# Performance work log

Hardware: AMD Instinct MI355X
Metric: run time of the kernel (lower is better)

Reference implementation:

```python
import jax, jax.numpy as jnp
import numpy as np

B, CIN, COUT, K, SDIM, H, W = 16, 512, 512, 3, 512, 64, 64


def setup_inputs() -> dict:
    key = jax.random.key(0)
    k1, k2, k3, k4 = jax.random.split(key, 4)
    return {
        "x": jax.random.normal(k1, (B, CIN, H, W), dtype=jnp.float32),
        "style": jax.random.normal(k2, (B, SDIM), dtype=jnp.float32),
        "weight": jax.random.normal(k3, (COUT, CIN, K, K), dtype=jnp.float32),
        "style_w": jax.random.normal(k4, (CIN, SDIM), dtype=jnp.float32),
        "style_b": jnp.ones((CIN,), dtype=jnp.float32),  # bias.data.fill_(1.0)
    }


def reference(x, style, weight, style_w, style_b):
    batch, in_ch, h, w_size = x.shape
    out_ch, _, ks, _ = weight.shape
    pad = ks // 2
    # EqualizedLinear: runtime weight scaling by 1/sqrt(fan_in)
    lin_scale = 1.0 / np.sqrt(style_w.shape[1])
    s = style @ (style_w * lin_scale).T + style_b  # [B, Cin]
    # modulate
    conv_scale = 1.0 / np.sqrt(in_ch * ks * ks)
    wmod = (weight[None] * conv_scale) * s[:, None, :, None, None]  # [B,Cout,Cin,k,k]
    # demodulate
    dcoef = jax.lax.rsqrt(jnp.sum(jnp.square(wmod), axis=(2, 3, 4)) + 1e-8)  # [B,Cout]
    wmod = wmod * dcoef[:, :, None, None, None]
    # grouped conv with groups = batch
    x_r = x.reshape(1, batch * in_ch, h, w_size)
    w_r = wmod.reshape(batch * out_ch, in_ch, ks, ks)
    out = jax.lax.conv_general_dilated(
        x_r, w_r,
        window_strides=(1, 1),
        padding=[(pad, pad), (pad, pad)],
        dimension_numbers=("NCHW", "OIHW", "NCHW"),
        feature_group_count=batch,
    )
    return out.reshape(batch, out_ch, h, w_size)
```

## Files before the change

### kernel.cpp

```cpp
#include <hip/hip_runtime.h>
#include <math.h>

#define B 16
#define CIN 512
#define COUT 512
#define SDIM 512
#define H 64
#define W 64

typedef short s16x8 __attribute__((ext_vector_type(8)));
typedef float f32x4 __attribute__((ext_vector_type(4)));

__device__ __constant__ float LIN_SCALE  = 0.04419417382415922f;
__device__ __constant__ float CONV_SCALE = 0.014731391274719742f;

__device__ __forceinline__ ushort f2bf(float f) {
  unsigned u = __float_as_uint(f);
  return (ushort)((u + 0x7FFFu + ((u >> 16) & 1u)) >> 16);
}

#define GLOAD16(g, l)                                           \
  __builtin_amdgcn_global_load_lds(                             \
      (const __attribute__((address_space(1))) unsigned*)(g),   \
      (__attribute__((address_space(3))) unsigned*)(l), 16, 0, 0)

__global__ __launch_bounds__(512) void style_mod_kernel(
    const float* __restrict__ style, const float* __restrict__ style_w,
    const float* __restrict__ style_b, float* __restrict__ s,
    float* __restrict__ s2) {
  const int b = blockIdx.x;
  const int ci = threadIdx.x;
  __shared__ float st[SDIM];
  st[ci] = style[b * SDIM + ci];
  __syncthreads();

  const float4* wr = reinterpret_cast<const float4*>(style_w + (size_t)ci * SDIM);
  float acc = 0.f;
#pragma unroll 4
  for (int k = 0; k < SDIM / 4; ++k) {
    float4 wv = wr[k];
    acc += st[4 * k + 0] * wv.x + st[4 * k + 1] * wv.y +
           st[4 * k + 2] * wv.z + st[4 * k + 3] * wv.w;
  }
  float v = acc * LIN_SCALE + style_b[ci];
  s[b * CIN + ci] = v;
  s2[b * CIN + ci] = v * v;
}

__global__ __launch_bounds__(256) void wsq_kernel(
    const float* __restrict__ weight, float* __restrict__ wsq) {
  const int i = blockIdx.x * blockDim.x + threadIdx.x;
  if (i >= COUT * CIN) return;
  const float* p = weight + (size_t)i * 9;
  float a = 0.f;
#pragma unroll
  for (int k = 0; k < 9; ++k) {
    float v = p[k];
    a += v * v;
  }
  wsq[i] = a;
}

__global__ __launch_bounds__(512) void dcoef_kernel(
    const float* __restrict__ s2, const float* __restrict__ wsq,
    float* __restrict__ outscale) {
  const int b = blockIdx.x;
  const int co = threadIdx.x;
  __shared__ float sh[CIN];
  sh[co] = s2[b * CIN + co];
  __syncthreads();

  const float4* wr = reinterpret_cast<const float4*>(wsq + (size_t)co * CIN);
  float acc = 0.f;
#pragma unroll 4
  for (int k = 0; k < CIN / 4; ++k) {
    float4 wv = wr[k];
    acc += sh[4 * k + 0] * wv.x + sh[4 * k + 1] * wv.y +
           sh[4 * k + 2] * wv.z + sh[4 * k + 3] * wv.w;
  }
  float d = rsqrtf(acc * CONV_SCALE * CONV_SCALE + 1e-8f);
  outscale[b * COUT + co] = d * CONV_SCALE;
}

__global__ __launch_bounds__(256) void pack_w_kernel(
    const float* __restrict__ w, ushort* __restrict__ wt) {
  const int t = blockIdx.x * 256 + threadIdx.x;
  const int s = t & 3;
  const int chunk = (t >> 2) & 15;
  const int co = t >> 6;
  const float4* wp =
      (const float4*)(w + ((size_t)co * 512 + chunk * 32 + s * 8) * 9);
  float wv[72];
#pragma unroll
  for (int i = 0; i < 18; ++i) {
    float4 v = wp[i];
    wv[4 * i + 0] = v.x; wv[4 * i + 1] = v.y;
    wv[4 * i + 2] = v.z; wv[4 * i + 3] = v.w;
  }
  const int sp = s ^ ((co >> 1) & 3);
  ushort* dst = wt + (size_t)chunk * 147456 + (size_t)co * 32 + sp * 8;
#pragma unroll
  for (int j = 0; j < 9; ++j) {
    s16x8 p;
#pragma unroll
    for (int i = 0; i < 8; ++i) p[i] = (short)f2bf(wv[i * 9 + j]);
    *(s16x8*)(dst + (size_t)j * 16384) = p;
  }
}

__global__ __launch_bounds__(256) void pack_x_kernel(
    const float* __restrict__ x, const float* __restrict__ smod,
    ushort* __restrict__ xp) {
  __shared__ float xt[32][65];
  __shared__ float sm[32];
  const int tid = threadIdx.x;
  const int gr = blockIdx.x, chunk = blockIdx.y, b = blockIdx.z;
  if (tid < 32) sm[tid] = smod[b * 512 + chunk * 32 + tid];
  {
    const int ci = tid >> 3, cq = tid & 7;
    const float4* rp = (const float4*)(
        x + (((size_t)b * 512 + chunk * 32 + ci) * 64 + gr) * 64 + cq * 8);
    float4 a = rp[0], c2 = rp[1];
    float* row = &xt[ci][cq * 8];
    row[0] = a.x; row[1] = a.y; row[2] = a.z; row[3] = a.w;
    row[4] = c2.x; row[5] = c2.y; row[6] = c2.z; row[7] = c2.w;
  }
  __syncthreads();
  const int c = tid >> 2, s = tid & 3;
  s16x8 p;
#pragma unroll
  for (int i = 0; i < 8; ++i)
    p[i] = (short)f2bf(xt[s * 8 + i][c] * sm[s * 8 + i]);
  const int sp = s ^ (((c + 1) >> 1) & 3);
  *(s16x8*)(xp + ((size_t)(b * 16 + chunk) * 64 + gr) * 2048 + c * 32 + sp * 8) = p;
}

__global__ __launch_bounds__(256, 2) void conv_mfma2_kernel(
    const ushort* __restrict__ wt, const ushort* __restrict__ xp,
    const float* __restrict__ outscale, float* __restrict__ out) {
  __shared__ ushort ws[9][64][32];
  __shared__ ushort xs[6][66][32];

  const int tid = threadIdx.x;
  const int hb = blockIdx.x, cb = blockIdx.y, b = blockIdx.z;
  const int h0 = hb * 4, co0 = cb * 64;
  const int lane = tid & 63, wid = tid >> 6;
  const int l15 = lane & 15, l4 = lane >> 4;

  {
    s16x8* p = (s16x8*)&xs[0][0][0];
    for (int e = tid; e < 1584; e += 256) p[e] = (s16x8)0;
  }

  f32x4 acc[4][4];
#pragma unroll
  for (int mt = 0; mt < 4; ++mt)
#pragma unroll
    for (int nt = 0; nt < 4; ++nt) acc[mt][nt] = (f32x4)0.f;

  const int am = (l4 ^ ((l15 >> 1) & 3)) * 16;
  int aoff[4];
#pragma unroll
  for (int mt = 0; mt < 4; ++mt) aoff[mt] = (mt * 16 + l15) * 64 + am;
  int boff[12];
#pragma unroll
  for (int nt = 0; nt < 4; ++nt)
#pragma unroll
    for (int kw = 0; kw < 3; ++kw) {
      int col = nt * 16 + l15 + kw;
      boff[nt * 3 + kw] =
          wid * 4224 + col * 64 + ((l4 ^ ((col >> 1) & 3)) * 16);
    }

  const char* wsrc0 = (const char*)wt + cb * 4096 + wid * 1024 + lane * 16;
  const char* xsrc0 =
      (const char*)xp + (size_t)b * 4194304 + wid * 1024 + lane * 16;
  char* wdst = (char*)&ws[0][0][0] + wid * 1024 + lane * 16;
  char* xdst = (char*)&xs[0][0][0] + 64 + wid * 1024 + lane * 16;

  __syncthreads();

  for (int chunk = 0; chunk < 16; ++chunk) {
    const char* wsrc = wsrc0 + chunk * 294912;
    const char* xsrc = xsrc0 + chunk * 262144;
#pragma unroll
    for (int t = 0; t < 9; ++t)
      GLOAD16(wsrc + t * 32768, wdst + t * 4096);
#pragma unroll
    for (int t = 0; t < 6; ++t) {
      int gr = h0 - 1 + t;
      if ((unsigned)gr < 64u) GLOAD16(xsrc + gr * 4096, xdst + t * 4224);
    }
    __syncthreads();

#pragma unroll
    for (int kh = 0; kh < 3; ++kh) {
      const char* xrow = (const char*)&xs[0][0][0] + kh * 4224;
#pragma unroll
      for (int kw = 0; kw < 3; ++kw) {
        const int j = kh * 3 + kw;
        const char* wj = (const char*)&ws[0][0][0] + j * 4096;
        s16x8 af[4], bf[4];
#pragma unroll
        for (int mt = 0; mt < 4; ++mt)
          af[mt] = *(const s16x8*)(wj + aoff[mt]);
#pragma unroll
        for (int nt = 0; nt < 4; ++nt)
          bf[nt] = *(const s16x8*)(xrow + boff[nt * 3 + kw]);
#pragma unroll
        for (int mt = 0; mt < 4; ++mt)
#pragma unroll
          for (int nt = 0; nt < 4; ++nt)
            acc[mt][nt] = __builtin_amdgcn_mfma_f32_16x16x32_bf16(
                af[mt], bf[nt], acc[mt][nt], 0, 0, 0);
      }
    }
    __syncthreads();
  }

  const int h = h0 + wid;
#pragma unroll
  for (int mt = 0; mt < 4; ++mt) {
#pragma unroll
    for (int r = 0; r < 4; ++r) {
      const int co = co0 + mt * 16 + l4 * 4 + r;
      const float osc = outscale[b * COUT + co];
      float* orow = out + (((size_t)b * COUT + co) * H + h) * W;
#pragma unroll
      for (int nt = 0; nt < 4; ++nt)
        orow[nt * 16 + l15] = acc[mt][nt][r] * osc;
    }
  }
}

__global__ __launch_bounds__(256, 2) void conv_mfma_kernel(
    const float* __restrict__ x, const float* __restrict__ weight,
    const float* __restrict__ s, const float* __restrict__ outscale,
    float* __restrict__ out) {
  __shared__ ushort xs[6][66][32];
  __shared__ ushort ws[9][64][32];

  const int tid = threadIdx.x;
  const int hb = blockIdx.x;
  const int cb = blockIdx.y;
  const int b  = blockIdx.z;
  const int h0 = hb * 4;
  const int co0 = cb * 64;
  const int lane = tid & 63;
  const int wid = tid >> 6;
  const int l15 = lane & 15;
  const int l4  = lane >> 4;

  f32x4 acc[4][4];
#pragma unroll
  for (int mt = 0; mt < 4; ++mt)
#pragma unroll
    for (int nt = 0; nt < 4; ++nt) acc[mt][nt] = (f32x4)0.f;

  const int wq = tid & 3;
  const int wco = tid >> 2;

  for (int c0 = 0; c0 < CIN; c0 += 32) {
    {
      const float4* wp = reinterpret_cast<const float4*>(
          weight + ((size_t)(co0 + wco) * CIN + c0 + wq * 8) * 9);
      float wv[72];
#pragma unroll
      for (int t = 0; t < 18; ++t) {
        float4 v = wp[t];
        wv[4 * t + 0] = v.x; wv[4 * t + 1] = v.y;
        wv[4 * t + 2] = v.z; wv[4 * t + 3] = v.w;
      }
      float sv[8];
#pragma unroll
      for (int i = 0; i < 8; ++i) sv[i] = s[b * CIN + c0 + wq * 8 + i];
#pragma unroll
      for (int j = 0; j < 9; ++j) {
        s16x8 p;
#pragma unroll
        for (int i = 0; i < 8; ++i)
          p[i] = (short)f2bf(wv[i * 9 + j] * sv[i]);
        *reinterpret_cast<s16x8*>(&ws[j][wco][wq * 8]) = p;
      }
    }
#pragma unroll
    for (int it = 0; it < 7; ++it) {
      int e = tid + it * 256;
      if (e < 6 * 66 * 4) {
        int q = e & 3;
        int t2 = e >> 2;
        int cc = t2 % 66;
        int r = t2 / 66;
        int gr = h0 - 1 + r;
        int gc = cc - 1;
        s16x8 p;
        if ((unsigned)gr < H && (unsigned)gc < W) {
          const float* xp2 =
              x + (((size_t)b * CIN + c0 + q * 8) * H + gr) * W + gc;
#pragma unroll
          for (int i = 0; i < 8; ++i) p[i] = (short)f2bf(xp2[(size_t)i * H * W]);
        } else {
#pragma unroll
          for (int i = 0; i < 8; ++i) p[i] = 0;
        }
        *reinterpret_cast<s16x8*>(&xs[r][cc][q * 8]) = p;
      }
    }
    __syncthreads();

#pragma unroll
    for (int kh = 0; kh < 3; ++kh) {
#pragma unroll
      for (int kw = 0; kw < 3; ++kw) {
        const int j = kh * 3 + kw;
        s16x8 af[4], bf[4];
#pragma unroll
        for (int mt = 0; mt < 4; ++mt)
          af[mt] = *reinterpret_cast<const s16x8*>(
              &ws[j][mt * 16 + l15][l4 * 8]);
#pragma unroll
        for (int nt = 0; nt < 4; ++nt)
          bf[nt] = *reinterpret_cast<const s16x8*>(
              &xs[wid + kh][nt * 16 + l15 + kw][l4 * 8]);
#pragma unroll
        for (int mt = 0; mt < 4; ++mt)
#pragma unroll
          for (int nt = 0; nt < 4; ++nt)
            acc[mt][nt] = __builtin_amdgcn_mfma_f32_16x16x32_bf16(
                af[mt], bf[nt], acc[mt][nt], 0, 0, 0);
      }
    }
    __syncthreads();
  }

  const int h = h0 + wid;
#pragma unroll
  for (int mt = 0; mt < 4; ++mt) {
#pragma unroll
    for (int r = 0; r < 4; ++r) {
      const int co = co0 + mt * 16 + l4 * 4 + r;
      const float osc = outscale[b * COUT + co];
      float* orow = out + (((size_t)b * COUT + co) * H + h) * W;
#pragma unroll
      for (int nt = 0; nt < 4; ++nt)
        orow[nt * 16 + l15] = acc[mt][nt][r] * osc;
    }
  }
}

extern "C" void kernel_launch(void* const* d_in, const int* in_sizes, int n_in,
                              void* d_out, int out_size, void* d_ws,
                              size_t ws_size, hipStream_t stream) {
  const float* x = (const float*)d_in[0];
  const float* style = (const float*)d_in[1];
  const float* weight = (const float*)d_in[2];
  const float* style_w = (const float*)d_in[3];
  const float* style_b = (const float*)d_in[4];
  float* out = (float*)d_out;

  char* wsb = (char*)d_ws;
  float* s = (float*)(wsb + 0);
  float* s2 = (float*)(wsb + 32768);
  float* wsq = (float*)(wsb + 65536);
  float* outscale = (float*)(wsb + 1114112);
  ushort* wt = (ushort*)(wsb + 1146880);
  ushort* xp = (ushort*)(wsb + 5865472);
  const size_t NEED = 72974336;

  style_mod_kernel<<<B, 512, 0, stream>>>(style, style_w, style_b, s, s2);
  wsq_kernel<<<(COUT * CIN + 255) / 256, 256, 0, stream>>>(weight, wsq);
  dcoef_kernel<<<B, 512, 0, stream>>>(s2, wsq, outscale);

  if (ws_size >= NEED) {
    pack_w_kernel<<<128, 256, 0, stream>>>(weight, wt);
    pack_x_kernel<<<dim3(64, 16, 16), 256, 0, stream>>>(x, s, xp);
    conv_mfma2_kernel<<<dim3(16, 8, 16), 256, 0, stream>>>(wt, xp, outscale,
                                                           out);
  } else {
    conv_mfma_kernel<<<dim3(16, 8, 16), 256, 0, stream>>>(x, weight, s,
                                                          outscale, out);
  }
}
```

Before: 343.7 us.

## Add double-buffered 8-row conv kernel with async LDS loads

Adds a new conv kernel using 512-thread blocks that each cover 8 output rows. It double-buffers weight and input tiles in about 158KB of dynamic LDS, so async global-to-LDS loads of the next channel chunk overlap the MFMA work on the current one. It also doubles weight reuse per block and opts in to the larger LDS size through a function attribute. The pack kernels now always run and the fp32 fallback kernel is removed, so a small workspace is no longer handled safely, and the large LDS footprint limits each CU to one block.

```diff
diff --git a/kernel.cpp b/kernel.cpp
--- a/kernel.cpp
+++ b/kernel.cpp
@@ -135,6 +135,124 @@
   *(s16x8*)(xp + ((size_t)(b * 16 + chunk) * 64 + gr) * 2048 + c * 32 + sp * 8) = p;
 }
 
+#define WSBUF 36864
+#define XSBUF 42240
+#define XSOFF 73728
+
+__global__ __launch_bounds__(512, 2) void conv_mfma3_kernel(
+    const ushort* __restrict__ wt, const ushort* __restrict__ xp,
+    const float* __restrict__ outscale, float* __restrict__ out) {
+  extern __shared__ char smem[];
+
+  const int tid = threadIdx.x;
+  const int hb = blockIdx.x;
+  const int cb = blockIdx.y;
+  const int b  = blockIdx.z;
+  const int h0 = hb * 8, co0 = cb * 64;
+  const int lane = tid & 63, wid = tid >> 6;
+  const int l15 = lane & 15, l4 = lane >> 4;
+
+  {
+    s16x8* p = (s16x8*)(smem + XSOFF);
+    for (int e = tid; e < (2 * XSBUF) / 16; e += 512) p[e] = (s16x8)0;
+  }
+
+  f32x4 acc[4][4];
+#pragma unroll
+  for (int mt = 0; mt < 4; ++mt)
+#pragma unroll
+    for (int nt = 0; nt < 4; ++nt) acc[mt][nt] = (f32x4)0.f;
+
+  const int am = (l4 ^ ((l15 >> 1) & 3)) * 16;
+  int aoff[4];
+#pragma unroll
+  for (int mt = 0; mt < 4; ++mt) aoff[mt] = (mt * 16 + l15) * 64 + am;
+  int boff[12];
+#pragma unroll
+  for (int nt = 0; nt < 4; ++nt)
+#pragma unroll
+    for (int kw = 0; kw < 3; ++kw) {
+      int col = nt * 16 + l15 + kw;
+      boff[nt * 3 + kw] =
+          wid * 4224 + col * 64 + ((l4 ^ ((col >> 1) & 3)) * 16);
+    }
+
+  const char* wsrc0 = (const char*)wt + cb * 4096 + lane * 16;
+  const char* xsrc0 = (const char*)xp + (size_t)b * 4194304 + lane * 16;
+
+  __syncthreads();
+
+  auto stage = [&](int chunk, int buf) {
+    const char* wsrc = wsrc0 + (size_t)chunk * 294912;
+    const char* xsrc = xsrc0 + (size_t)chunk * 262144;
+    char* wdst = smem + buf * WSBUF + lane * 16;
+    char* xdst = smem + XSOFF + buf * XSBUF + 64 + lane * 16;
+    for (int e = wid; e < 76; e += 8) {
+      if (e < 36) {
+        int j = e >> 2, q = e & 3;
+        GLOAD16(wsrc + j * 32768 + q * 1024, wdst + j * 4096 + q * 1024);
+      } else {
+        int r = (e - 36) >> 2, q = (e - 36) & 3;
+        int gr = h0 - 1 + r;
+        if ((unsigned)gr < 64u)
+          GLOAD16(xsrc + (size_t)gr * 4096 + q * 1024,
+                  xdst + r * 4224 + q * 1024);
+      }
+    }
+  };
+
+  auto compute = [&](int buf) {
+    const char* wb = smem + buf * WSBUF;
+    const char* xb = smem + XSOFF + buf * XSBUF;
+#pragma unroll
+    for (int kh = 0; kh < 3; ++kh) {
+      const char* xrow = xb + kh * 4224;
+#pragma unroll
+      for (int kw = 0; kw < 3; ++kw) {
+        const int j = kh * 3 + kw;
+        const char* wj = wb + j * 4096;
+        s16x8 af[4], bf[4];
+#pragma unroll
+        for (int mt = 0; mt < 4; ++mt)
+          af[mt] = *(const s16x8*)(wj + aoff[mt]);
+#pragma unroll
+        for (int nt = 0; nt < 4; ++nt)
+          bf[nt] = *(const s16x8*)(xrow + boff[nt * 3 + kw]);
+#pragma unroll
+        for (int mt = 0; mt < 4; ++mt)
+#pragma unroll
+          for (int nt = 0; nt < 4; ++nt)
+            acc[mt][nt] = __builtin_amdgcn_mfma_f32_16x16x32_bf16(
+                af[mt], bf[nt], acc[mt][nt], 0, 0, 0);
+      }
+    }
+  };
+
+  stage(0, 0);
+  for (int c = 0; c < 16; c += 2) {
+    __syncthreads();
+    if (c + 1 < 16) stage(c + 1, 1);
+    compute(0);
+    __syncthreads();
+    if (c + 2 < 16) stage(c + 2, 0);
+    compute(1);
+  }
+
+  const int h = h0 + wid;
+#pragma unroll
+  for (int mt = 0; mt < 4; ++mt) {
+#pragma unroll
+    for (int r = 0; r < 4; ++r) {
+      const int co = co0 + mt * 16 + l4 * 4 + r;
+      const float osc = outscale[b * COUT + co];
+      float* orow = out + (((size_t)b * COUT + co) * H + h) * W;
+#pragma unroll
+      for (int nt = 0; nt < 4; ++nt)
+        orow[nt * 16 + l15] = acc[mt][nt][r] * osc;
+    }
+  }
+}
+
 __global__ __launch_bounds__(256, 2) void conv_mfma2_kernel(
     const ushort* __restrict__ wt, const ushort* __restrict__ xp,
     const float* __restrict__ outscale, float* __restrict__ out) {
@@ -207,121 +325,6 @@
 #pragma unroll
         for (int nt = 0; nt < 4; ++nt)
           bf[nt] = *(const s16x8*)(xrow + boff[nt * 3 + kw]);
-#pragma unroll
-        for (int mt = 0; mt < 4; ++mt)
-#pragma unroll
-          for (int nt = 0; nt < 4; ++nt)
-            acc[mt][nt] = __builtin_amdgcn_mfma_f32_16x16x32_bf16(
-                af[mt], bf[nt], acc[mt][nt], 0, 0, 0);
-      }
-    }
-    __syncthreads();
-  }
-
-  const int h = h0 + wid;
-#pragma unroll
-  for (int mt = 0; mt < 4; ++mt) {
-#pragma unroll
-    for (int r = 0; r < 4; ++r) {
-      const int co = co0 + mt * 16 + l4 * 4 + r;
-      const float osc = outscale[b * COUT + co];
-      float* orow = out + (((size_t)b * COUT + co) * H + h) * W;
-#pragma unroll
-      for (int nt = 0; nt < 4; ++nt)
-        orow[nt * 16 + l15] = acc[mt][nt][r] * osc;
-    }
-  }
-}
-
-__global__ __launch_bounds__(256, 2) void conv_mfma_kernel(
-    const float* __restrict__ x, const float* __restrict__ weight,
-    const float* __restrict__ s, const float* __restrict__ outscale,
-    float* __restrict__ out) {
-  __shared__ ushort xs[6][66][32];
-  __shared__ ushort ws[9][64][32];
-
-  const int tid = threadIdx.x;
-  const int hb = blockIdx.x;
-  const int cb = blockIdx.y;
-  const int b  = blockIdx.z;
-  const int h0 = hb * 4;
-  const int co0 = cb * 64;
-  const int lane = tid & 63;
-  const int wid = tid >> 6;
-  const int l15 = lane & 15;
-  const int l4  = lane >> 4;
-
-  f32x4 acc[4][4];
-#pragma unroll
-  for (int mt = 0; mt < 4; ++mt)
-#pragma unroll
-    for (int nt = 0; nt < 4; ++nt) acc[mt][nt] = (f32x4)0.f;
-
-  const int wq = tid & 3;
-  const int wco = tid >> 2;
-
-  for (int c0 = 0; c0 < CIN; c0 += 32) {
-    {
-      const float4* wp = reinterpret_cast<const float4*>(
-          weight + ((size_t)(co0 + wco) * CIN + c0 + wq * 8) * 9);
-      float wv[72];
-#pragma unroll
-      for (int t = 0; t < 18; ++t) {
-        float4 v = wp[t];
-        wv[4 * t + 0] = v.x; wv[4 * t + 1] = v.y;
-        wv[4 * t + 2] = v.z; wv[4 * t + 3] = v.w;
-      }
-      float sv[8];
-#pragma unroll
-      for (int i = 0; i < 8; ++i) sv[i] = s[b * CIN + c0 + wq * 8 + i];
-#pragma unroll
-      for (int j = 0; j < 9; ++j) {
-        s16x8 p;
-#pragma unroll
-        for (int i = 0; i < 8; ++i)
-          p[i] = (short)f2bf(wv[i * 9 + j] * sv[i]);
-        *reinterpret_cast<s16x8*>(&ws[j][wco][wq * 8]) = p;
-      }
-    }
-#pragma unroll
-    for (int it = 0; it < 7; ++it) {
-      int e = tid + it * 256;
-      if (e < 6 * 66 * 4) {
-        int q = e & 3;
-        int t2 = e >> 2;
-        int cc = t2 % 66;
-        int r = t2 / 66;
-        int gr = h0 - 1 + r;
-        int gc = cc - 1;
-        s16x8 p;
-        if ((unsigned)gr < H && (unsigned)gc < W) {
-          const float* xp2 =
-              x + (((size_t)b * CIN + c0 + q * 8) * H + gr) * W + gc;
-#pragma unroll
-          for (int i = 0; i < 8; ++i) p[i] = (short)f2bf(xp2[(size_t)i * H * W]);
-        } else {
-#pragma unroll
-          for (int i = 0; i < 8; ++i) p[i] = 0;
-        }
-        *reinterpret_cast<s16x8*>(&xs[r][cc][q * 8]) = p;
-      }
-    }
-    __syncthreads();
-
-#pragma unroll
-    for (int kh = 0; kh < 3; ++kh) {
-#pragma unroll
-      for (int kw = 0; kw < 3; ++kw) {
-        const int j = kh * 3 + kw;
-        s16x8 af[4], bf[4];
-#pragma unroll
-        for (int mt = 0; mt < 4; ++mt)
-          af[mt] = *reinterpret_cast<const s16x8*>(
-              &ws[j][mt * 16 + l15][l4 * 8]);
-#pragma unroll
-        for (int nt = 0; nt < 4; ++nt)
-          bf[nt] = *reinterpret_cast<const s16x8*>(
-              &xs[wid + kh][nt * 16 + l15 + kw][l4 * 8]);
 #pragma unroll
         for (int mt = 0; mt < 4; ++mt)
 #pragma unroll
@@ -371,13 +374,20 @@
   wsq_kernel<<<(COUT * CIN + 255) / 256, 256, 0, stream>>>(weight, wsq);
   dcoef_kernel<<<B, 512, 0, stream>>>(s2, wsq, outscale);
 
-  if (ws_size >= NEED) {
-    pack_w_kernel<<<128, 256, 0, stream>>>(weight, wt);
-    pack_x_kernel<<<dim3(64, 16, 16), 256, 0, stream>>>(x, s, xp);
+  pack_w_kernel<<<128, 256, 0, stream>>>(weight, wt);
+  pack_x_kernel<<<dim3(64, 16, 16), 256, 0, stream>>>(x, s, xp);
+
+  const int DLDS = 2 * WSBUF + 2 * XSBUF;
+  static_assert(2 * WSBUF + 2 * XSBUF == 158208, "lds layout");
+  hipError_t attr_ok = hipFuncSetAttribute(
+      reinterpret_cast<const void*>(conv_mfma3_kernel),
+      hipFuncAttributeMaxDynamicSharedMemorySize, DLDS);
+
+  if (attr_ok == hipSuccess && ws_size >= NEED) {
+    conv_mfma3_kernel<<<dim3(8, 8, 16), 512, DLDS, stream>>>(wt, xp, outscale,
+                                                             out);
+  } else {
     conv_mfma2_kernel<<<dim3(16, 8, 16), 256, 0, stream>>>(wt, xp, outscale,
                                                            out);
-  } else {
-    conv_mfma_kernel<<<dim3(16, 8, 16), 256, 0, stream>>>(x, weight, s,
-                                                          outscale, out);
-  }
-}
+  }
+}
```

Result: slower. 363.6 us (+5.8%).
